# Optimization experiments

Hardware: AMD Instinct MI355X
Metric: run time of the kernel (lower is better)

The kernel has to match this reference:

```python
import jax, jax.numpy as jnp
import numpy as np

N_ARY = 4
H_SIZE = 512
X_SIZE = 512
DEPTH = 9
N_NODES = (N_ARY ** DEPTH - 1) // (N_ARY - 1)  # 87381, complete 4-ary tree, BFS numbering


def setup_inputs() -> dict:
    key = jax.random.key(0)
    ks = jax.random.split(key, 7)
    x = jax.random.normal(ks[0], (N_NODES, X_SIZE), jnp.float32)
    # torch nn.Linear convention: y = x @ W.T + b, W:[out, in]
    Ww = jax.random.normal(ks[1], (H_SIZE, X_SIZE), jnp.float32) * (X_SIZE ** -0.5)
    Wb = jax.random.normal(ks[2], (H_SIZE,), jnp.float32) * 0.01
    Uzr_w = jax.random.normal(ks[3], (2 * H_SIZE, N_ARY * H_SIZE), jnp.float32) * ((N_ARY * H_SIZE) ** -0.5)
    Uzr_b = jax.random.normal(ks[4], (2 * H_SIZE,), jnp.float32) * 0.01
    Uh_w = jax.random.normal(ks[5], (H_SIZE, N_ARY * H_SIZE), jnp.float32) * ((N_ARY * H_SIZE) ** -0.5)
    Uh_b = jax.random.normal(ks[6], (H_SIZE,), jnp.float32) * 0.01
    return {"x": x, "Ww": Ww, "Wb": Wb, "Uzr_w": Uzr_w, "Uzr_b": Uzr_b,
            "Uh_w": Uh_w, "Uh_b": Uh_b, "depth": DEPTH}


def reference(x, Ww, Wb, Uzr_w, Uzr_b, Uh_w, Uh_b, depth):
    n_ary = N_ARY
    h_size = Ww.shape[0]
    # initial state for every node; leaves keep it, internal nodes get overwritten
    h = jnp.tanh(x @ Ww.T + Wb)  # [N, H]
    # level l occupies indices [starts[l], starts[l+1]); level 0 is the root
    starts = [(n_ary ** l - 1) // (n_ary - 1) for l in range(depth + 1)]
    # process internal levels leaves-first (deepest internal level -> root)
    for l in range(depth - 2, -1, -1):
        s, e = starts[l], starts[l + 1]
        ids = np.arange(s, e)
        child = ids[:, None] * n_ary + 1 + np.arange(n_ary)[None, :]  # [m, n_ary]
        hc = h[child]                                  # gather children: [m, n_ary, H]
        m = e - s
        h_cat = hc.reshape(m, n_ary * h_size)          # mailbox concat (full arity -> no pad)
        zr = h_cat @ Uzr_w.T + Uzr_b                   # [m, 2H]
        z = jax.nn.sigmoid(zr[:, :h_size])
        r = jax.nn.sigmoid(zr[:, h_size:])
        h_cand = jnp.tanh((jnp.tile(r, (1, n_ary)) * h_cat) @ Uh_w.T + Uh_b)
        h_new = hc.sum(axis=1) * z + (1.0 - z) * h_cand
        h = h.at[s:e].set(h_new)                       # scatter level update
    return h
```

## Files before the change

kernel.cpp:

```cpp
#include <hip/hip_runtime.h>
#include <math.h>

#define H 512
typedef unsigned short u16;
typedef __attribute__((ext_vector_type(8))) short bf16x8;
typedef __attribute__((ext_vector_type(4))) float f32x4;
typedef __attribute__((ext_vector_type(8))) unsigned short u16x8;

constexpr int LEAF0  = 21845;
constexpr int NLEAF  = 65536;
constexpr int NNODES = 87381;

__device__ __forceinline__ u16 f2b(float f) {
    union { float f; unsigned u; } v; v.f = f;
    unsigned r = v.u + 0x7fffu + ((v.u >> 16) & 1u);
    return (u16)(r >> 16);
}
__device__ __forceinline__ float b2f(u16 b) {
    union { unsigned u; float f; } v; v.u = ((unsigned)b) << 16; return v.f;
}
__device__ __forceinline__ float sigm(float x) {
    return __fdividef(1.f, 1.f + __expf(-x));
}
__device__ __forceinline__ float ftanh(float x) {
    float e = __expf(-2.f * fabsf(x));
    float r = __fdividef(1.f - e, 1.f + e);
    return copysignf(r, x);
}

template<int N> __device__ __forceinline__ void vmwait() {
    if constexpr (N == 0)       asm volatile("s_waitcnt vmcnt(0)" ::: "memory");
    else if constexpr (N == 2)  asm volatile("s_waitcnt vmcnt(2)" ::: "memory");
    else if constexpr (N == 3)  asm volatile("s_waitcnt vmcnt(3)" ::: "memory");
    else if constexpr (N == 4)  asm volatile("s_waitcnt vmcnt(4)" ::: "memory");
    else if constexpr (N == 6)  asm volatile("s_waitcnt vmcnt(6)" ::: "memory");
    else if constexpr (N == 8)  asm volatile("s_waitcnt vmcnt(8)" ::: "memory");
    else                        asm volatile("s_waitcnt vmcnt(16)" ::: "memory");
}

__device__ __forceinline__ void gload16(const u16* g, u16* l) {
    __builtin_amdgcn_global_load_lds(
        (const __attribute__((address_space(1))) void*)g,
        (__attribute__((address_space(3))) void*)l, 16, 0, 0);
}

template<int EPI, int NC, int WC>
__device__ __forceinline__ void epi_vec(
    const f32x4* va, int gr, int gc0,
    float* __restrict__ outf, u16* __restrict__ outb,
    u16* __restrict__ zrb, const u16* auxl, int lrow, int coffs, int outRow0)
{
    constexpr int NV = NC / 8;
    if constexpr (EPI == 1) {
        f32x4 ov[NC/4]; u16x8 hv[NV];
#pragma unroll
        for (int i = 0; i < NC; ++i) {
            float v = ftanh(va[i>>2][i&3]);
            ov[i>>2][i&3] = v; hv[i>>3][i&7] = f2b(v);
        }
        size_t o = (size_t)(outRow0 + gr) * H + gc0;
#pragma unroll
        for (int j = 0; j < NC/4; ++j) *(f32x4*)&outf[o + 4*j] = ov[j];
#pragma unroll
        for (int j = 0; j < NV; ++j) *(u16x8*)&outb[o + 8*j] = hv[j];
    } else if constexpr (EPI == 0) {
        auto aux_read = [&](int ch, int jj) -> u16x8 {
            int cr  = 4*lrow + ch;
            int key = (cr >> 2) & (WC/8 - 1);
            int j   = (coffs >> 3) + jj;
            return *(const u16x8*)&auxl[cr*WC + ((j ^ key) << 3)];
        };
        if (gc0 < H) {
            u16x8 zv[NV]; f32x4 hs[NC/4];
#pragma unroll
            for (int i = 0; i < NC; ++i) {
                zv[i>>3][i&7] = f2b(sigm(va[i>>2][i&3]));
                hs[i>>2][i&3] = 0.f;
            }
#pragma unroll
            for (int ch = 0; ch < 4; ++ch) {
#pragma unroll
                for (int j = 0; j < NV; ++j) {
                    u16x8 cv = aux_read(ch, j);
#pragma unroll
                    for (int k = 0; k < 8; ++k) {
                        int i = 8*j + k;
                        hs[i>>2][i&3] += b2f(cv[k]);
                    }
                }
            }
            u16x8 sv[NV];
#pragma unroll
            for (int i = 0; i < NC; ++i) sv[i>>3][i&7] = f2b(hs[i>>2][i&3]);
            size_t zo = (size_t)gr * 1024 + gc0;
#pragma unroll
            for (int j = 0; j < NV; ++j) *(u16x8*)&zrb[zo + 8*j] = zv[j];
#pragma unroll
            for (int j = 0; j < NV; ++j) *(u16x8*)&zrb[zo + H + 8*j] = sv[j];
        } else {
            f32x4 rr[NC/4];
#pragma unroll
            for (int i = 0; i < NC; ++i) rr[i>>2][i&3] = sigm(va[i>>2][i&3]);
            const int cc = gc0 - H;
#pragma unroll
            for (int ch = 0; ch < 4; ++ch) {
#pragma unroll
                for (int j = 0; j < NV; ++j) {
                    u16x8 cv = aux_read(ch, j);
                    u16x8 ov;
#pragma unroll
                    for (int k = 0; k < 8; ++k) {
                        int i = 8*j + k;
                        ov[k] = f2b(rr[i>>2][i&3] * b2f(cv[k]));
                    }
                    *(u16x8*)&outb[(size_t)gr*2048 + ch*H + cc + 8*j] = ov;
                }
            }
        }
    } else {
        size_t zo = (size_t)gr * 1024 + gc0;
        u16x8 zv[NV], sv[NV];
#pragma unroll
        for (int j = 0; j < NV; ++j) zv[j] = *(const u16x8*)&zrb[zo + 8*j];
#pragma unroll
        for (int j = 0; j < NV; ++j) sv[j] = *(const u16x8*)&zrb[zo + H + 8*j];
        f32x4 ov[NC/4]; u16x8 hv[NV];
#pragma unroll
        for (int i = 0; i < NC; ++i) {
            float hc = ftanh(va[i>>2][i&3]);
            float z  = b2f(zv[i>>3][i&7]);
            float v  = b2f(sv[i>>3][i&7]) * z + (1.f - z) * hc;
            ov[i>>2][i&3] = v; hv[i>>3][i&7] = f2b(v);
        }
        size_t o = (size_t)(outRow0 + gr) * H + gc0;
#pragma unroll
        for (int j = 0; j < NC/4; ++j) *(f32x4*)&outf[o + 4*j] = ov[j];
#pragma unroll
        for (int j = 0; j < NV; ++j) *(u16x8*)&outb[o + 8*j] = hv[j];
    }
}

template<int WC>
__device__ __forceinline__ void stage_aux(
    u16* wls, const u16* auxg, int lane)
{
    constexpr int UPW = WC / 8;
    constexpr int NIT = 64 * UPW / 64;
#pragma unroll
    for (int it = 0; it < NIT; ++it) {
        int row = (it * 64 + lane) / UPW;
        int sp  = (lane & (UPW - 1)) ^ ((row >> 2) & (UPW - 1));
        gload16(auxg + row * H + sp * 8, &wls[it * 512]);
    }
}

__global__ void cvt_all(const float* __restrict__ s0, u16* __restrict__ d0, int n0,
                        const float* __restrict__ s1, u16* __restrict__ d1, int n1,
                        const float* __restrict__ s2, u16* __restrict__ d2, int n2,
                        const float* __restrict__ s3, u16* __restrict__ d3, int n3)
{
    int i = blockIdx.x * blockDim.x + threadIdx.x;
    int st = gridDim.x * blockDim.x;
    int tot = n0 + n1 + n2 + n3;
    for (; i < tot; i += st) {
        const float* s; u16* d; int k = i;
        if (k < n0)      { s = s0; d = d0; }
        else { k -= n0;
        if (k < n1)      { s = s1; d = d1; }
        else { k -= n1;
        if (k < n2)      { s = s2; d = d2; }
        else { k -= n2;    s = s3; d = d3; } } }
        float4 v = ((const float4*)s)[k];
        ushort4 o;
        o.x = f2b(v.x); o.y = f2b(v.y); o.z = f2b(v.z); o.w = f2b(v.w);
        ((ushort4*)d)[k] = o;
    }
}

template<int EPI>
__global__ __launch_bounds__(512, 2) void gemm8p(
    const u16* __restrict__ A, int lda, int M, int K,
    const u16* __restrict__ Bm,
    const float* __restrict__ bias,
    float* __restrict__ outf,
    u16*  __restrict__ outb,
    u16*  __restrict__ zrb,
    const u16* __restrict__ auxb,
    int outRow0)
{
    constexpr int MI = 4, NI = 4;
    constexpr int AH = 256 * 32;
    constexpr int BH = 128 * 32;
    constexpr int L  = 3;

    __shared__ __align__(16) char smem[(4 * AH + 4 * BH) * 2];
    u16* Asm = reinterpret_cast<u16*>(smem);
    u16* Bsm = reinterpret_cast<u16*>(smem) + 4 * AH;

    const int tid  = threadIdx.x;
    const int lane = tid & 63;
    const int wave = tid >> 6;
    const int wm = wave >> 1;
    const int wn = wave & 1;

    int bx, by;
    {
        const int gx = gridDim.x, gy = gridDim.y;
        int p = blockIdx.y * gx + blockIdx.x;
        if ((gy & 7) == 0) {
            int xcd = p & 7, slot = p >> 3;
            bx = slot % gx;
            by = (slot / gx) * 8 + xcd;
        } else { bx = blockIdx.x; by = blockIdx.y; }
    }
    const int row0 = by * 256;
    const int col0 = bx * 128;

    const u16 *gA0, *gA1, *gB;
    int ldsA0, ldsA1, ldsB;
    {
        int e8 = tid, row = e8 >> 2, jc = e8 & 3, js = jc ^ ((row >> 1) & 3);
        gA0 = A + (size_t)(row0 + row) * lda + js * 8;  ldsA0 = e8 * 8;
        int e9 = 512 + tid, row2 = e9 >> 2, jc2 = e9 & 3,
            js2 = jc2 ^ ((row2 >> 1) & 3);
        gA1 = A + (size_t)(row0 + row2) * lda + js2 * 8; ldsA1 = e9 * 8;
        int br = tid >> 2, bjc = tid & 3, bjs = bjc ^ ((br >> 1) & 3);
        gB = Bm + (size_t)(col0 + br) * K + bjs * 8;     ldsB = tid * 8;
    }
    auto stage = [&](int slot) {
        gload16(gA0, &Asm[slot * AH + ldsA0]); gA0 += 32;
        gload16(gA1, &Asm[slot * AH + ldsA1]); gA1 += 32;
        gload16(gB,  &Bsm[slot * BH + ldsB]);  gB  += 32;
    };

    const int rl = lane & 15;
    const int qq = lane >> 4;
    const int ua   = qq ^ ((rl >> 1) & 3);
    const int aoff = (wm * 64 + rl) * 32 + ua * 8;
    const int boff = (wn * 64 + rl) * 32 + ua * 8;

    auto ld_frags = [&](int h, bf16x8 (&fa)[MI], bf16x8 (&fb)[NI]) {
        const u16* aB = Asm + (h & 3) * AH + aoff;
        const u16* bB = Bsm + (h & 3) * BH + boff;
#pragma unroll
        for (int mi = 0; mi < MI; ++mi)
            fa[mi] = *(const bf16x8*)(aB + mi * 512);
#pragma unroll
        for (int ni = 0; ni < NI; ++ni)
            fb[ni] = *(const bf16x8*)(bB + ni * 512);
    };

    f32x4 acc[MI][NI] = {};
    const int nh = K / 32;
    bf16x8 fa0[MI], fb0[NI], fa1[MI], fb1[NI];

    stage(0); stage(1); stage(2);
    vmwait<2 * L>();
    __builtin_amdgcn_s_barrier();
    asm volatile("" ::: "memory");
    ld_frags(0, fa0, fb0);

    auto iter = [&](int h, bf16x8 (&cfa)[MI], bf16x8 (&cfb)[NI],
                           bf16x8 (&nfa)[MI], bf16x8 (&nfb)[NI]) {
        if (h + 2 < nh) vmwait<L>();
        else            vmwait<0>();
        __builtin_amdgcn_s_barrier();
        asm volatile("" ::: "memory");
        if (h + 3 < nh) stage((h + 3) & 3);
        if (h + 1 < nh) ld_frags(h + 1, nfa, nfb);
        __builtin_amdgcn_s_setprio(1);
#pragma unroll
        for (int mi = 0; mi < MI; ++mi)
#pragma unroll
            for (int ni = 0; ni < NI; ++ni)
                acc[mi][ni] = __builtin_amdgcn_mfma_f32_16x16x32_bf16(
                    cfa[mi], cfb[ni], acc[mi][ni], 0, 0, 0);
        __builtin_amdgcn_s_setprio(0);
    };

    for (int h = 0; h < nh; h += 2) {
        iter(h,     fa0, fb0, fa1, fb1);
        iter(h + 1, fa1, fb1, fa0, fb0);
    }

    float bcol[NI];
#pragma unroll
    for (int ni = 0; ni < NI; ++ni)
        bcol[ni] = bias[col0 + wn * 64 + ni * 16 + rl];

    __syncthreads();
    char* wreg = smem + wave * 8192;
    float* Csw = reinterpret_cast<float*>(wreg);
    u16*   wls = reinterpret_cast<u16*>(wreg);
    const int rq  = lane >> 4;
    const int rl2 = lane & 15;
#pragma unroll
    for (int mi = 0; mi < MI; ++mi) {
#pragma unroll
        for (int ni = 0; ni < NI; ++ni)
#pragma unroll
            for (int q = 0; q < 4; ++q)
                Csw[(rq*4 + q)*68 + ni*16 + rl2] = acc[mi][ni][q] + bcol[ni];
        asm volatile("s_waitcnt lgkmcnt(0)" ::: "memory");
        f32x4 va[4];
#pragma unroll
        for (int j = 0; j < 4; ++j)
            va[j] = *(const f32x4*)&Csw[rl2*68 + rq*16 + 4*j];
        if constexpr (EPI == 0) {
            asm volatile("s_waitcnt lgkmcnt(0)" ::: "memory");
            int c0 = ((col0 < H) ? col0 : col0 - H) + wn * 64;
            const u16* auxg = auxb + (size_t)(4*(row0 + wm*64 + mi*16)) * H + c0;
            stage_aux<64>(wls, auxg, lane);
            vmwait<0>();
        }
        int gr  = row0 + wm*64 + mi*16 + rl2;
        int gc0 = col0 + wn*64 + rq*16;
        if (gr < M)
            epi_vec<EPI, 16, 64>(va, gr, gc0, outf, outb, zrb, wls, rl2, rq*16, outRow0);
    }
}

template<int EPI>
__global__ __launch_bounds__(512) void gemm512(
    const u16* __restrict__ A, int lda, int M, int K,
    const u16* __restrict__ Bm,
    const float* __restrict__ bias,
    float* __restrict__ outf,
    u16*  __restrict__ outb,
    u16*  __restrict__ zrb,
    const u16* __restrict__ auxb,
    int outRow0)
{
    __shared__ __align__(16) char smem[4*128*32*2 * 2];
    u16* Asm = reinterpret_cast<u16*>(smem);
    u16* Bsm = reinterpret_cast<u16*>(smem) + 4 * 128 * 32;

    const int tid  = threadIdx.x;
    const int lane = tid & 63;
    const int wave = tid >> 6;
    const int wm = wave >> 2;
    const int wn = wave & 3;

    int bx, by;
    {
        const int gx = gridDim.x, gy = gridDim.y;
        int p = blockIdx.y * gx + blockIdx.x;
        if ((gy & 7) == 0) {
            int xcd = p & 7, slot = p >> 3;
            bx = slot % gx;
            by = (slot / gx) * 8 + xcd;
        } else { bx = blockIdx.x; by = blockIdx.y; }
    }
    const int row0 = by * 128;
    const int col0 = bx * 128;

    const u16 *gA, *gB;
    int ldsE;
    {
        int row = tid >> 2, jc = tid & 3, js = jc ^ ((row >> 1) & 3);
        gA = A  + (size_t)(row0 + row) * lda + js * 8;
        gB = Bm + (size_t)(col0 + row) * K   + js * 8;
        ldsE = tid * 8;
    }
    auto stage = [&](int b) {
        gload16(gA, &Asm[b * (128*32) + ldsE]); gA += 32;
        gload16(gB, &Bsm[b * (128*32) + ldsE]); gB += 32;
    };

    const int rl = lane & 15;
    const int qq = lane >> 4;
    const int ua   = qq ^ ((rl >> 1) & 3);
    const int aoff = (wm * 64 + rl) * 32 + ua * 8;
    const int boff = (wn * 32 + rl) * 32 + ua * 8;

    f32x4 acc[4][2] = {};
    const int nt = K / 32;
    stage(0);
    stage(1);

    for (int t = 0; t < nt; ++t) {
        if (t + 2 < nt) {
            stage((t + 2) & 3);
            vmwait<4>();
        } else if (t + 2 == nt) {
            vmwait<2>();
        } else {
            vmwait<0>();
        }
        __builtin_amdgcn_s_barrier();
        asm volatile("" ::: "memory");

        const u16* aB = Asm + (t & 3) * (128*32) + aoff;
        const u16* bB = Bsm + (t & 3) * (128*32) + boff;
        bf16x8 af[4], bfr[2];
#pragma unroll
        for (int mi = 0; mi < 4; ++mi)
            af[mi] = *(const bf16x8*)(aB + mi * 512);
#pragma unroll
        for (int ni = 0; ni < 2; ++ni)
            bfr[ni] = *(const bf16x8*)(bB + ni * 512);
#pragma unroll
        for (int mi = 0; mi < 4; ++mi)
#pragma unroll
            for (int ni = 0; ni < 2; ++ni)
                acc[mi][ni] = __builtin_amdgcn_mfma_f32_16x16x32_bf16(
                    af[mi], bfr[ni], acc[mi][ni], 0, 0, 0);
    }

    float bcol[2];
#pragma unroll
    for (int ni = 0; ni < 2; ++ni)
        bcol[ni] = bias[col0 + wn * 32 + ni * 16 + rl];

    __syncthreads();
    char* wreg = smem + wave * 8192;
    float* Csw = reinterpret_cast<float*>(wreg);
    u16*   wls = reinterpret_cast<u16*>(wreg);
    const int rq  = lane >> 4;
    const int rl2 = lane & 15;
#pragma unroll
    for (int mi = 0; mi < 4; ++mi) {
#pragma unroll
        for (int ni = 0; ni < 2; ++ni)
#pragma unroll
            for (int q = 0; q < 4; ++q)
                Csw[(rq*4 + q)*36 + ni*16 + rl2] = acc[mi][ni][q] + bcol[ni];
        asm volatile("s_waitcnt lgkmcnt(0)" ::: "memory");
        f32x4 va[2];
#pragma unroll
        for (int j = 0; j < 2; ++j)
            va[j] = *(const f32x4*)&Csw[rl2*36 + rq*8 + 4*j];
        if constexpr (EPI == 0) {
            asm volatile("s_waitcnt lgkmcnt(0)" ::: "memory");
            int c0 = ((col0 < H) ? col0 : col0 - H) + wn * 32;
            const u16* auxg = auxb + (size_t)(4*(row0 + wm*64 + mi*16)) * H + c0;
            stage_aux<32>(wls, auxg, lane);
            vmwait<0>();
        }
        int gr  = row0 + wm*64 + mi*16 + rl2;
        int gc0 = col0 + wn*32 + rq*8;
        if (gr < M)
            epi_vec<EPI, 8, 32>(va, gr, gc0, outf, outb, zrb, wls, rl2, rq*8, outRow0);
    }
}

template<int EPI>
__global__ __launch_bounds__(256, 1) void gemm_sk(
    const u16* __restrict__ A, int lda, int M, int K,
    const u16* __restrict__ Bm,
    const float* __restrict__ bias,
    float* __restrict__ outf,
    u16*  __restrict__ outb,
    u16*  __restrict__ zrb,
    const u16* __restrict__ auxb,
    int outRow0)
{
    __shared__ __align__(16) char smem[98304];
    u16* ring = reinterpret_cast<u16*>(smem);

    const int tid  = threadIdx.x;
    const int lane = tid & 63;
    const int wave = tid >> 6;
    const int row0 = blockIdx.y * 64;
    const int col0 = blockIdx.x * 64;
    const int KC   = K >> 2;
    const int kb0  = wave * KC;
    const int NS   = KC / 32;

    u16* wring = ring + wave * 12288;

    auto stage = [&](int sl, int kt) {
        u16* As = wring + sl * 4096;
        u16* Bs = As + 2048;
#pragma unroll
        for (int it = 0; it < 4; ++it) {
            int e8  = it * 64 + lane;
            int row = e8 >> 2;
            int jc  = e8 & 3;
            int js  = jc ^ ((row >> 1) & 3);
            int ar = row0 + row; if (ar >= M) ar = M - 1;
            gload16(A + (size_t)ar * lda + kt + js * 8, &As[e8 * 8]);
            gload16(Bm + (size_t)(col0 + row) * K + kt + js * 8, &Bs[e8 * 8]);
        }
    };

    const int rl = lane & 15;
    const int qq = lane >> 4;
    const int ua   = qq ^ ((rl >> 1) & 3);
    const int aoff = rl * 32 + ua * 8;

    f32x4 acc[4][4] = {};
    stage(0, kb0);
    stage(1, kb0 + 32);

    for (int s = 0; s < NS; ++s) {
        if (s + 2 < NS) { stage((s + 2) % 3, kb0 + (s + 2) * 32); vmwait<16>(); }
        else if (s + 1 < NS) vmwait<8>();
        else                 vmwait<0>();
        asm volatile("" ::: "memory");
        const u16* As = wring + (s % 3) * 4096;
        const u16* Bs = As + 2048;
        bf16x8 af[4], bfr[4];
#pragma unroll
        for (int mi = 0; mi < 4; ++mi)
            af[mi] = *(const bf16x8*)&As[aoff + mi * 512];
#pragma unroll
        for (int ni = 0; ni < 4; ++ni)
            bfr[ni] = *(const bf16x8*)&Bs[aoff + ni * 512];
#pragma unroll
        for (int mi = 0; mi < 4; ++mi)
#pragma unroll
            for (int ni = 0; ni < 4; ++ni)
                acc[mi][ni] = __builtin_amdgcn_mfma_f32_16x16x32_bf16(
                    af[mi], bfr[ni], acc[mi][ni], 0, 0, 0);
    }

    __syncthreads();
    float* P  = reinterpret_cast<float*>(smem);
    float* Pw = P + wave * 4096;
    const int rq = lane >> 4;
#pragma unroll
    for (int mi = 0; mi < 4; ++mi)
#pragma unroll
        for (int ni = 0; ni < 4; ++ni)
#pragma unroll
            for (int q = 0; q < 4; ++q)
                Pw[(mi*16 + rq*4 + q) * 64 + ni*16 + rl] = acc[mi][ni][q];
    asm volatile("s_waitcnt lgkmcnt(0)" ::: "memory");
    __syncthreads();

    u16* auxl = reinterpret_cast<u16*>(smem + 65536);
    if constexpr (EPI == 0) {
        int c0 = (col0 < H) ? col0 : col0 - H;
        const u16* auxg = auxb + (size_t)(4 * row0) * H + c0;
        const int maxr = 4 * (M - row0);
#pragma unroll
        for (int it = 0; it < 8; ++it) {
            int e   = it * 256 + tid;
            int row = e >> 3;
            int crow = row; if (crow >= maxr) crow = maxr - 1;
            int sp  = (e & 7) ^ ((row >> 2) & 7);
            gload16(auxg + (size_t)crow * H + sp * 8, &auxl[e * 8]);
        }
    }

    const int orow = tid >> 2;
    const int cq   = tid & 3;
    f32x4 va[4];
#pragma unroll
    for (int j = 0; j < 4; ++j) {
        f32x4 v = *(const f32x4*)&P[orow*64 + cq*16 + 4*j];
#pragma unroll
        for (int w = 1; w < 4; ++w)
            v += *(const f32x4*)&P[w*4096 + orow*64 + cq*16 + 4*j];
        v += *(const f32x4*)&bias[col0 + cq*16 + 4*j];
        va[j] = v;
    }
    if constexpr (EPI == 0) vmwait<0>();
    asm volatile("s_waitcnt lgkmcnt(0)" ::: "memory");
    int gr = row0 + orow;
    if (gr < M)
        epi_vec<EPI, 16, 64>(va, gr, col0 + cq*16, outf, outb, zrb,
                             auxl, orow, cq*16, outRow0);
}

extern "C" void kernel_launch(void* const* d_in, const int* in_sizes, int n_in,
                              void* d_out, int out_size, void* d_ws, size_t ws_size,
                              hipStream_t stream) {
    const float* x     = (const float*)d_in[0];
    const float* Ww    = (const float*)d_in[1];
    const float* Wb    = (const float*)d_in[2];
    const float* Uzr_w = (const float*)d_in[3];
    const float* Uzr_b = (const float*)d_in[4];
    const float* Uh_w  = (const float*)d_in[5];
    const float* Uh_b  = (const float*)d_in[6];
    float* out = (float*)d_out;

    char* ws = (char*)d_ws;
    size_t off = 0;
    u16* hb   = (u16*)(ws + off); off += (size_t)NNODES * H * 2;
    u16* zr   = (u16*)(ws + off); off += (size_t)16384 * 1024 * 2;
    u16* rhxb = (u16*)(ws + off); off += (size_t)16384 * 2048 * 2;
    u16* Wwb  = (u16*)(ws + off); off += (size_t)512 * 512 * 2;
    u16* Uzrb = (u16*)(ws + off); off += (size_t)1024 * 2048 * 2;
    u16* Uhb  = (u16*)(ws + off); off += (size_t)512 * 2048 * 2;

    cvt_all<<<dim3(8192), 256, 0, stream>>>(
        Ww, Wwb, 512 * 512 / 4,
        Uzr_w, Uzrb, 1024 * 2048 / 4,
        Uh_w, Uhb, 512 * 2048 / 4,
        x + (size_t)LEAF0 * H, rhxb, NLEAF * H / 4);

    gemm8p<1><<<dim3(H / 128, NLEAF / 256), 512, 0, stream>>>(
        rhxb, H, NLEAF, H, Wwb, Wb, out, hb, nullptr, nullptr, LEAF0);

    static const int pow4[9] = {1, 4, 16, 64, 256, 1024, 4096, 16384, 65536};
    int starts[10]; starts[0] = 0;
    for (int l = 0; l < 9; ++l) starts[l + 1] = starts[l] + pow4[l];

    for (int l = 7; l >= 0; --l) {
        int s = starts[l], m = pow4[l];
        int cs = 4 * s + 1;
        if (m >= 16384) {
            gemm8p<0><<<dim3(1024 / 128, m / 256), 512, 0, stream>>>(
                hb + (size_t)cs * H, 2048, m, 2048, Uzrb, Uzr_b,
                nullptr, rhxb, zr, hb + (size_t)cs * H, 0);
            gemm8p<2><<<dim3(H / 128, m / 256), 512, 0, stream>>>(
                rhxb, 2048, m, 2048, Uhb, Uh_b,
                out, hb, zr, nullptr, s);
        } else if (m >= 4096) {
            int gm = (m + 127) / 128;
            gemm512<0><<<dim3(1024 / 128, gm), 512, 0, stream>>>(
                hb + (size_t)cs * H, 2048, m, 2048, Uzrb, Uzr_b,
                nullptr, rhxb, zr, hb + (size_t)cs * H, 0);
            gemm512<2><<<dim3(H / 128, gm), 512, 0, stream>>>(
                rhxb, 2048, m, 2048, Uhb, Uh_b,
                out, hb, zr, nullptr, s);
        } else {
            int gm = (m + 63) / 64;
            gemm_sk<0><<<dim3(1024 / 64, gm), 256, 0, stream>>>(
                hb + (size_t)cs * H, 2048, m, 2048, Uzrb, Uzr_b,
                nullptr, rhxb, zr, hb + (size_t)cs * H, 0);
            gemm_sk<2><<<dim3(512 / 64, gm), 256, 0, stream>>>(
                rhxb, 2048, m, 2048, Uhb, Uh_b,
                out, hb, zr, nullptr, s);
        }
    }
}
```

Before: 483.1 us.

## Add 256x256-tile GEMM kernel for leaf projection and large zr levels

```diff
diff --git a/kernel.cpp b/kernel.cpp
--- a/kernel.cpp
+++ b/kernel.cpp
@@ -29,13 +29,14 @@
 }
 
 template<int N> __device__ __forceinline__ void vmwait() {
-    if constexpr (N == 0)       asm volatile("s_waitcnt vmcnt(0)" ::: "memory");
-    else if constexpr (N == 2)  asm volatile("s_waitcnt vmcnt(2)" ::: "memory");
-    else if constexpr (N == 3)  asm volatile("s_waitcnt vmcnt(3)" ::: "memory");
-    else if constexpr (N == 4)  asm volatile("s_waitcnt vmcnt(4)" ::: "memory");
-    else if constexpr (N == 6)  asm volatile("s_waitcnt vmcnt(6)" ::: "memory");
-    else if constexpr (N == 8)  asm volatile("s_waitcnt vmcnt(8)" ::: "memory");
-    else                        asm volatile("s_waitcnt vmcnt(16)" ::: "memory");
+    if constexpr (N == 0)        asm volatile("s_waitcnt vmcnt(0)" ::: "memory");
+    else if constexpr (N == 2)   asm volatile("s_waitcnt vmcnt(2)" ::: "memory");
+    else if constexpr (N == 3)   asm volatile("s_waitcnt vmcnt(3)" ::: "memory");
+    else if constexpr (N == 4)   asm volatile("s_waitcnt vmcnt(4)" ::: "memory");
+    else if constexpr (N == 6)   asm volatile("s_waitcnt vmcnt(6)" ::: "memory");
+    else if constexpr (N == 8)   asm volatile("s_waitcnt vmcnt(8)" ::: "memory");
+    else if constexpr (N == 16)  asm volatile("s_waitcnt vmcnt(16)" ::: "memory");
+    else                         asm volatile("s_waitcnt vmcnt(0)" ::: "memory");
 }
 
 __device__ __forceinline__ void gload16(const u16* g, u16* l) {
@@ -178,6 +179,139 @@
 }
 
 template<int EPI>
+__global__ __launch_bounds__(512, 2) void gemm2c(
+    const u16* __restrict__ A, int lda, int M, int K,
+    const u16* __restrict__ Bm,
+    const float* __restrict__ bias,
+    float* __restrict__ outf,
+    u16*  __restrict__ outb,
+    u16*  __restrict__ zrb,
+    const u16* __restrict__ auxb,
+    int outRow0)
+{
+    constexpr int MI = 8, NI = 4;
+    constexpr int AH = 256 * 32;
+    constexpr int BH = 256 * 32;
+    constexpr int L  = 4;
+
+    __shared__ __align__(16) char smem[4 * (AH + BH) * 2];
+    u16* Asm = reinterpret_cast<u16*>(smem);
+    u16* Bsm = reinterpret_cast<u16*>(smem) + 4 * AH;
+
+    const int tid  = threadIdx.x;
+    const int lane = tid & 63;
+    const int wave = tid >> 6;
+    const int wm = wave >> 2;
+    const int wn = wave & 3;
+
+    int bx, by;
+    {
+        const int gx = gridDim.x, gy = gridDim.y;
+        int p = blockIdx.y * gx + blockIdx.x;
+        if ((gy & 7) == 0) {
+            int xcd = p & 7, slot = p >> 3;
+            bx = slot % gx;
+            by = (slot / gx) * 8 + xcd;
+        } else { bx = blockIdx.x; by = blockIdx.y; }
+    }
+    const int row0 = by * 256;
+    const int col0 = bx * 256;
+
+    const u16 *gA0, *gA1, *gB0, *gB1;
+    int lA0, lA1, lB0, lB1;
+    {
+        int e8 = tid, row = e8 >> 2, jc = e8 & 3, js = jc ^ ((row >> 1) & 3);
+        gA0 = A  + (size_t)(row0 + row) * lda + js * 8;  lA0 = e8 * 8;
+        gB0 = Bm + (size_t)(col0 + row) * K   + js * 8;  lB0 = e8 * 8;
+        int e9 = 512 + tid, row2 = e9 >> 2, jc2 = e9 & 3,
+            js2 = jc2 ^ ((row2 >> 1) & 3);
+        gA1 = A  + (size_t)(row0 + row2) * lda + js2 * 8; lA1 = e9 * 8;
+        gB1 = Bm + (size_t)(col0 + row2) * K   + js2 * 8; lB1 = e9 * 8;
+    }
+    auto stage = [&](int slot) {
+        gload16(gA0, &Asm[slot * AH + lA0]); gA0 += 32;
+        gload16(gA1, &Asm[slot * AH + lA1]); gA1 += 32;
+        gload16(gB0, &Bsm[slot * BH + lB0]); gB0 += 32;
+        gload16(gB1, &Bsm[slot * BH + lB1]); gB1 += 32;
+    };
+
+    const int rl = lane & 15;
+    const int qq = lane >> 4;
+    const int ua   = qq ^ ((rl >> 1) & 3);
+    const int aoff = (wm * 128 + rl) * 32 + ua * 8;
+    const int boff = (wn * 64  + rl) * 32 + ua * 8;
+
+    f32x4 acc[MI][NI] = {};
+    const int nh = K / 32;
+
+    stage(0); stage(1); stage(2);
+
+    for (int h = 0; h < nh; ++h) {
+        const int rem = nh - h;
+        if (rem >= 3)      vmwait<2 * L>();
+        else if (rem == 2) vmwait<L>();
+        else               vmwait<0>();
+        __builtin_amdgcn_s_barrier();
+        asm volatile("" ::: "memory");
+        if (h + 3 < nh) stage((h + 3) & 3);
+
+        const u16* aB = Asm + (h & 3) * AH + aoff;
+        const u16* bB = Bsm + (h & 3) * BH + boff;
+        bf16x8 fa[MI], fb[NI];
+#pragma unroll
+        for (int mi = 0; mi < MI; ++mi)
+            fa[mi] = *(const bf16x8*)(aB + mi * 512);
+#pragma unroll
+        for (int ni = 0; ni < NI; ++ni)
+            fb[ni] = *(const bf16x8*)(bB + ni * 512);
+        __builtin_amdgcn_s_setprio(1);
+#pragma unroll
+        for (int mi = 0; mi < MI; ++mi)
+#pragma unroll
+            for (int ni = 0; ni < NI; ++ni)
+                acc[mi][ni] = __builtin_amdgcn_mfma_f32_16x16x32_bf16(
+                    fa[mi], fb[ni], acc[mi][ni], 0, 0, 0);
+        __builtin_amdgcn_s_setprio(0);
+    }
+
+    float bcol[NI];
+#pragma unroll
+    for (int ni = 0; ni < NI; ++ni)
+        bcol[ni] = bias[col0 + wn * 64 + ni * 16 + rl];
+
+    __syncthreads();
+    char* wreg = smem + wave * 8192;
+    float* Csw = reinterpret_cast<float*>(wreg);
+    u16*   wls = reinterpret_cast<u16*>(wreg);
+    const int rq  = lane >> 4;
+    const int rl2 = lane & 15;
+#pragma unroll
+    for (int mi = 0; mi < MI; ++mi) {
+#pragma unroll
+        for (int ni = 0; ni < NI; ++ni)
+#pragma unroll
+            for (int q = 0; q < 4; ++q)
+                Csw[(rq*4 + q)*68 + ni*16 + rl2] = acc[mi][ni][q] + bcol[ni];
+        asm volatile("s_waitcnt lgkmcnt(0)" ::: "memory");
+        f32x4 va[4];
+#pragma unroll
+        for (int j = 0; j < 4; ++j)
+            va[j] = *(const f32x4*)&Csw[rl2*68 + rq*16 + 4*j];
+        if constexpr (EPI == 0) {
+            asm volatile("s_waitcnt lgkmcnt(0)" ::: "memory");
+            int c0 = ((col0 < H) ? col0 : col0 - H) + wn * 64;
+            const u16* auxg = auxb + (size_t)(4*(row0 + wm*128 + mi*16)) * H + c0;
+            stage_aux<64>(wls, auxg, lane);
+            vmwait<0>();
+        }
+        int gr  = row0 + wm*128 + mi*16 + rl2;
+        int gc0 = col0 + wn*64 + rq*16;
+        if (gr < M)
+            epi_vec<EPI, 16, 64>(va, gr, gc0, outf, outb, zrb, wls, rl2, rq*16, outRow0);
+    }
+}
+
+template<int EPI>
 __global__ __launch_bounds__(512, 2) void gemm8p(
     const u16* __restrict__ A, int lda, int M, int K,
     const u16* __restrict__ Bm,
@@ -591,7 +725,7 @@
         Uh_w, Uhb, 512 * 2048 / 4,
         x + (size_t)LEAF0 * H, rhxb, NLEAF * H / 4);
 
-    gemm8p<1><<<dim3(H / 128, NLEAF / 256), 512, 0, stream>>>(
+    gemm2c<1><<<dim3(H / 256, NLEAF / 256), 512, 0, stream>>>(
         rhxb, H, NLEAF, H, Wwb, Wb, out, hb, nullptr, nullptr, LEAF0);
 
     static const int pow4[9] = {1, 4, 16, 64, 256, 1024, 4096, 16384, 65536};
@@ -602,7 +736,7 @@
         int s = starts[l], m = pow4[l];
         int cs = 4 * s + 1;
         if (m >= 16384) {
-            gemm8p<0><<<dim3(1024 / 128, m / 256), 512, 0, stream>>>(
+            gemm2c<0><<<dim3(1024 / 256, m / 256), 512, 0, stream>>>(
                 hb + (size_t)cs * H, 2048, m, 2048, Uzrb, Uzr_b,
                 nullptr, rhxb, zr, hb + (size_t)cs * H, 0);
             gemm8p<2><<<dim3(H / 128, m / 256), 512, 0, stream>>>(
```

Result: no change. 475.9 us, median of 2 (-1.5%).
